# Optimization experiments

Hardware: AMD Instinct MI355X
Metric: run time of the kernel (lower is better)

## Reference

```python
import jax, jax.numpy as jnp
import numpy as np

TOP_K = 2


def setup_inputs() -> dict:
    key = jax.random.key(0)
    ks = jax.random.split(key, 8)
    B, S, D, I, E = 4, 2048, 1024, 2048, 8
    scale = 0.02
    return {
        "hidden_states": jax.random.normal(ks[0], (B, S, D), dtype=jnp.float32),
        "router_w": jax.random.normal(ks[1], (D, E), dtype=jnp.float32) * scale,
        "router_b": jnp.zeros((E,), dtype=jnp.float32),
        "gate_w": jax.random.normal(ks[2], (E, D, I), dtype=jnp.float32) * scale,
        "gate_b": jnp.zeros((E, I), dtype=jnp.float32),
        "up_w": jax.random.normal(ks[3], (E, D, I), dtype=jnp.float32) * scale,
        "up_b": jnp.zeros((E, I), dtype=jnp.float32),
        "down_w": jax.random.normal(ks[4], (E, I, D), dtype=jnp.float32) * scale,
        "down_b": jnp.zeros((E, D), dtype=jnp.float32),
    }


def reference(hidden_states, router_w, router_b, gate_w, gate_b, up_w, up_b, down_w, down_b):
    B, S, D = hidden_states.shape
    E = router_w.shape[1]
    x = hidden_states.reshape(-1, D)  # [T, D]
    T = x.shape[0]

    # Router: softmax over experts, then top-k selection + renormalization
    logits = x @ router_w + router_b              # [T, E]
    probs = jax.nn.softmax(logits, axis=-1)       # [T, E]
    top_v, top_i = jax.lax.top_k(probs, TOP_K)    # [T, K]
    top_v = top_v / jnp.sum(top_v, axis=-1, keepdims=True)

    # Scatter renormalized probs to dense [T, E] combine weights (top-k indices are distinct)
    weights = jnp.zeros((T, E), dtype=x.dtype).at[jnp.arange(T)[:, None], top_i].set(top_v)

    # Dense expert SwiGLU: compute all experts, weighted combine (faithful math)
    gate = jnp.einsum('td,edi->eti', x, gate_w) + gate_b[:, None, :]   # [E, T, I]
    up = jnp.einsum('td,edi->eti', x, up_w) + up_b[:, None, :]         # [E, T, I]
    h = jax.nn.silu(gate) * up                                          # [E, T, I]
    expert_out = jnp.einsum('eti,eid->etd', h, down_w) + down_b[:, None, :]  # [E, T, D]

    y = jnp.einsum('te,etd->td', weights, expert_out)                   # [T, D]
    return y.reshape(B, S, D)
```

## Files before the change

### kernel.cpp

```cpp
#include <hip/hip_runtime.h>

#define T_TOK 8192
#define DDIM 1024
#define IDIM 2048
#define NEXP 8

typedef short bf16x8 __attribute__((ext_vector_type(8)));
typedef float f32x4 __attribute__((ext_vector_type(4)));

__device__ __forceinline__ unsigned short f2bf(float f) {
  union { float f; unsigned int u; } v; v.f = f;
  unsigned int r = v.u + 0x7fffu + ((v.u >> 16) & 1u);
  return (unsigned short)(r >> 16);
}
__device__ __forceinline__ float bf2f(unsigned short u) {
  union { unsigned int u; float f; } v; v.u = (unsigned int)u << 16;
  return v.f;
}

typedef const __attribute__((address_space(1))) void* gas_t;
typedef __attribute__((address_space(3))) void* las_t;
__device__ __forceinline__ void async_copy16(void* lds, const void* g) {
  __builtin_amdgcn_global_load_lds((gas_t)g, (las_t)lds, 16, 0, 0);
}

__global__ __launch_bounds__(256) void tconv_kernel(
    const float* __restrict__ src, ushort* __restrict__ dst, int R, int C,
    int sel, int interleave, size_t srcEStride, size_t dstEStride) {
  __shared__ ushort lt[64 * 72];
  const int e = blockIdx.z;
  const float* s = src + (size_t)e * srcEStride;
  ushort* d = dst + (size_t)e * dstEStride;
  const int c0 = blockIdx.x * 64, r0 = blockIdx.y * 64;
  const int t = threadIdx.x;
  const int tr = t >> 2;
  const int tc = (t & 3) * 16;
  const float* sp = s + (size_t)(r0 + tr) * C + c0 + tc;
  float4 v0 = ((const float4*)sp)[0];
  float4 v1 = ((const float4*)sp)[1];
  float4 v2 = ((const float4*)sp)[2];
  float4 v3 = ((const float4*)sp)[3];
#pragma unroll
  for (int j = 0; j < 4; ++j) lt[(tc + j) * 72 + tr]      = f2bf(((const float*)&v0)[j]);
#pragma unroll
  for (int j = 0; j < 4; ++j) lt[(tc + 4 + j) * 72 + tr]  = f2bf(((const float*)&v1)[j]);
#pragma unroll
  for (int j = 0; j < 4; ++j) lt[(tc + 8 + j) * 72 + tr]  = f2bf(((const float*)&v2)[j]);
#pragma unroll
  for (int j = 0; j < 4; ++j) lt[(tc + 12 + j) * 72 + tr] = f2bf(((const float*)&v3)[j]);
  __syncthreads();
  const int cr = t >> 2;
  const int seg = (t & 3) * 16;
  const int ci = c0 + cr;
  const int drow = interleave ? ((ci >> 6) * 128 + sel * 64 + (ci & 63)) : ci;
  uint4 o0 = *(const uint4*)&lt[cr * 72 + seg];
  uint4 o1 = *(const uint4*)&lt[cr * 72 + seg + 8];
  ushort* dp = d + (size_t)drow * R + r0 + seg;
  *(uint4*)dp = o0;
  *(uint4*)(dp + 8) = o1;
}

__global__ __launch_bounds__(256) void router_kernel(
    const float* __restrict__ x, const float* __restrict__ rw, const float* __restrict__ rb,
    int* __restrict__ cnt, int* __restrict__ lists, float* __restrict__ wts,
    int* __restrict__ pexp, ushort* __restrict__ xb) {
  __shared__ int tokE[128];
  __shared__ int loc[128];
  __shared__ int hist[NEXP];
  __shared__ int base[NEXP];
  const int tid = threadIdx.x;
  const int w = tid >> 6, lane = tid & 63;
  if (tid < NEXP) hist[tid] = 0;
  __syncthreads();

#pragma unroll 1
  for (int tt = 0; tt < 16; ++tt) {
    const int token = blockIdx.x * 64 + w * 16 + tt;
    float acc[NEXP];
#pragma unroll
    for (int e = 0; e < NEXP; ++e) acc[e] = 0.f;
    const float* xr = x + (size_t)token * DDIM;
    ushort* xbr = xb + (size_t)token * DDIM;
#pragma unroll
    for (int j = 0; j < DDIM / 64; ++j) {
      int d = j * 64 + lane;
      float xv = xr[d];
      xbr[d] = f2bf(xv);
      const float4* wp = (const float4*)(rw + d * NEXP);
      float4 w0 = wp[0], w1 = wp[1];
      acc[0] += xv * w0.x; acc[1] += xv * w0.y; acc[2] += xv * w0.z; acc[3] += xv * w0.w;
      acc[4] += xv * w1.x; acc[5] += xv * w1.y; acc[6] += xv * w1.z; acc[7] += xv * w1.w;
    }
#pragma unroll
    for (int e = 0; e < NEXP; ++e) {
      float v = acc[e];
      for (int off = 32; off > 0; off >>= 1) v += __shfl_xor(v, off, 64);
      acc[e] = v;
    }
    if (lane == 0) {
      float l[NEXP];
#pragma unroll
      for (int e = 0; e < NEXP; ++e) l[e] = acc[e] + rb[e];
      int i0 = 0; float b0 = l[0];
#pragma unroll
      for (int e = 1; e < NEXP; ++e) if (l[e] > b0) { b0 = l[e]; i0 = e; }
      int i1 = -1; float b1 = -3.0e38f;
#pragma unroll
      for (int e = 0; e < NEXP; ++e) if (e != i0 && l[e] > b1) { b1 = l[e]; i1 = e; }
      float e1 = expf(b1 - b0);
      float inv = 1.f / (1.f + e1);
      wts[token * 2 + 0] = inv;
      wts[token * 2 + 1] = e1 * inv;
      pexp[token * 2 + 0] = i0;
      pexp[token * 2 + 1] = i1;
      const int k = (w * 16 + tt) * 2;
      tokE[k] = i0;
      tokE[k + 1] = i1;
      loc[k] = atomicAdd(&hist[i0], 1);
      loc[k + 1] = atomicAdd(&hist[i1], 1);
    }
  }
  __syncthreads();
  if (tid < NEXP) base[tid] = atomicAdd(&cnt[tid], hist[tid]);
  __syncthreads();
  if (tid < 128) {
    const int e = tokE[tid];
    const int token = blockIdx.x * 64 + (tid >> 1);
    lists[e * T_TOK + base[e] + loc[tid]] = token * 2 + (tid & 1);
  }
}

__global__ __launch_bounds__(256, 2) void gemm1_kernel(
    const ushort* __restrict__ xb, const ushort* __restrict__ wcat,
    const float* __restrict__ gate_b, const float* __restrict__ up_b,
    const int* __restrict__ lists, const int* __restrict__ cnt,
    ushort* __restrict__ hbuf) {
  const int e = blockIdx.z;
  const int ce = cnt[e];
  const int p = blockIdx.x + (blockIdx.y << 5);
  const int l = (p & 7) * 128 + (p >> 3);
  const int m0 = (l & 31) * 256;
  const int by = l >> 5;
  if (m0 >= ce) return;

  __shared__ __align__(16) ushort smem[256 * 64 + 128 * 64];
  __shared__ int rowinfo[256];
  ushort* As = smem;
  ushort* Bs = smem + 256 * 64;

  const int tid = threadIdx.x;
  {
    int slot = m0 + tid;
    rowinfo[tid] = lists[e * T_TOK + (slot < ce ? slot : 0)];
  }
  __syncthreads();

  const int w = tid >> 6, lane = tid & 63;
  const int fm = lane & 15, fq = lane >> 4;
  const int lr = lane >> 3;
  const int lchunk = ((lane & 7) ^ lr) * 8;

  const ushort* wcatE = wcat + (size_t)e * 4096 * 1024;
  const ushort* aG[8]; const ushort* bG[4];
  ushort* aL[8]; ushort* bL[4];
#pragma unroll
  for (int j = 0; j < 8; ++j) {
    int rl = 64 * w + 8 * j + lr;
    aG[j] = xb + (size_t)(rowinfo[rl] >> 1) * DDIM + lchunk;
    aL[j] = As + (64 * w + 8 * j) * 64;
  }
#pragma unroll
  for (int j = 0; j < 4; ++j) {
    int rl = 32 * w + 8 * j + lr;
    bG[j] = wcatE + (size_t)(128 * by + rl) * DDIM + lchunk;
    bL[j] = Bs + (32 * w + 8 * j) * 64;
  }

  f32x4 acc[4][8];
  const f32x4 zero4 = {0.f, 0.f, 0.f, 0.f};
#pragma unroll
  for (int i = 0; i < 4; ++i)
#pragma unroll
    for (int j = 0; j < 8; ++j) acc[i][j] = zero4;

#pragma unroll 1
  for (int kt = 0; kt < DDIM / 64; ++kt) {
    __syncthreads();
#pragma unroll
    for (int j = 0; j < 8; ++j) async_copy16(aL[j], aG[j] + kt * 64);
#pragma unroll
    for (int j = 0; j < 4; ++j) async_copy16(bL[j], bG[j] + kt * 64);
    __syncthreads();
#pragma unroll
    for (int ks = 0; ks < 2; ++ks) {
      bf16x8 af[4], bfr[8];
#pragma unroll
      for (int mf = 0; mf < 4; ++mf) {
        int row = 64 * w + 16 * mf + fm;
        af[mf] = *(const bf16x8*)&As[row * 64 + (((ks * 4 + fq) ^ (fm & 7)) * 8)];
      }
#pragma unroll
      for (int nf = 0; nf < 8; ++nf) {
        int row = 16 * nf + fm;
        bfr[nf] = *(const bf16x8*)&Bs[row * 64 + (((ks * 4 + fq) ^ (fm & 7)) * 8)];
      }
#pragma unroll
      for (int mf = 0; mf < 4; ++mf)
#pragma unroll
        for (int nf = 0; nf < 8; ++nf)
          acc[mf][nf] = __builtin_amdgcn_mfma_f32_16x16x32_bf16(af[mf], bfr[nf], acc[mf][nf], 0, 0, 0);
    }
  }

#pragma unroll
  for (int mf = 0; mf < 4; ++mf) {
#pragma unroll
    for (int r = 0; r < 4; ++r) {
      const int row = 64 * w + 16 * mf + 4 * fq + r;
      if (m0 + row < ce) {
        const int packed = rowinfo[row];
#pragma unroll
        for (int nf = 0; nf < 4; ++nf) {
          const int col = 64 * by + 16 * nf + fm;
          float g = acc[mf][nf][r] + gate_b[e * IDIM + col];
          float u = acc[mf][nf + 4][r] + up_b[e * IDIM + col];
          float h = g * (1.f / (1.f + __expf(-g))) * u;
          hbuf[(size_t)packed * IDIM + col] = f2bf(h);
        }
      }
    }
  }
}

__global__ __launch_bounds__(256, 2) void gemm2_kernel(
    const ushort* __restrict__ hbuf, const ushort* __restrict__ downT,
    const int* __restrict__ lists, const int* __restrict__ cnt,
    ushort* __restrict__ cbuf) {
  const int e = blockIdx.z;
  const int ce = cnt[e];
  const int p = blockIdx.x + (blockIdx.y << 5);
  const int l = (p & 7) * 32 + (p >> 3);
  const int m0 = (l & 31) * 256;
  const int by = l >> 5;
  if (m0 >= ce) return;

  __shared__ __align__(16) ushort smem[256 * 64 + 128 * 64];
  __shared__ int rowinfo[256];
  ushort* As = smem;
  ushort* Bs = smem + 256 * 64;

  const int tid = threadIdx.x;
  {
    int slot = m0 + tid;
    rowinfo[tid] = lists[e * T_TOK + (slot < ce ? slot : 0)];
  }
  __syncthreads();

  const int w = tid >> 6, lane = tid & 63;
  const int fm = lane & 15, fq = lane >> 4;
  const int lr = lane >> 3;
  const int lchunk = ((lane & 7) ^ lr) * 8;

  const ushort* downE = downT + (size_t)e * DDIM * IDIM;
  const ushort* aG[8]; const ushort* bG[4];
  ushort* aL[8]; ushort* bL[4];
#pragma unroll
  for (int j = 0; j < 8; ++j) {
    int rl = 64 * w + 8 * j + lr;
    aG[j] = hbuf + (size_t)rowinfo[rl] * IDIM + lchunk;
    aL[j] = As + (64 * w + 8 * j) * 64;
  }
#pragma unroll
  for (int j = 0; j < 4; ++j) {
    int rl = 32 * w + 8 * j + lr;
    bG[j] = downE + (size_t)(128 * by + rl) * IDIM + lchunk;
    bL[j] = Bs + (32 * w + 8 * j) * 64;
  }

  f32x4 acc[4][8];
  const f32x4 zero4 = {0.f, 0.f, 0.f, 0.f};
#pragma unroll
  for (int i = 0; i < 4; ++i)
#pragma unroll
    for (int j = 0; j < 8; ++j) acc[i][j] = zero4;

#pragma unroll 1
  for (int kt = 0; kt < IDIM / 64; ++kt) {
    __syncthreads();
#pragma unroll
    for (int j = 0; j < 8; ++j) async_copy16(aL[j], aG[j] + kt * 64);
#pragma unroll
    for (int j = 0; j < 4; ++j) async_copy16(bL[j], bG[j] + kt * 64);
    __syncthreads();
#pragma unroll
    for (int ks = 0; ks < 2; ++ks) {
      bf16x8 af[4], bfr[8];
#pragma unroll
      for (int mf = 0; mf < 4; ++mf) {
        int row = 64 * w + 16 * mf + fm;
        af[mf] = *(const bf16x8*)&As[row * 64 + (((ks * 4 + fq) ^ (fm & 7)) * 8)];
      }
#pragma unroll
      for (int nf = 0; nf < 8; ++nf) {
        int row = 16 * nf + fm;
        bfr[nf] = *(const bf16x8*)&Bs[row * 64 + (((ks * 4 + fq) ^ (fm & 7)) * 8)];
      }
#pragma unroll
      for (int mf = 0; mf < 4; ++mf)
#pragma unroll
        for (int nf = 0; nf < 8; ++nf)
          acc[mf][nf] = __builtin_amdgcn_mfma_f32_16x16x32_bf16(af[mf], bfr[nf], acc[mf][nf], 0, 0, 0);
    }
  }

#pragma unroll
  for (int mf = 0; mf < 4; ++mf) {
#pragma unroll
    for (int r = 0; r < 4; ++r) {
      const int row = 64 * w + 16 * mf + 4 * fq + r;
      if (m0 + row < ce) {
        const int packed = rowinfo[row];
        ushort* crow = cbuf + (size_t)packed * DDIM + 128 * by;
#pragma unroll
        for (int nf = 0; nf < 8; ++nf)
          crow[16 * nf + fm] = f2bf(acc[mf][nf][r]);
      }
    }
  }
}

__global__ __launch_bounds__(256) void combine_kernel(
    const ushort* __restrict__ cbuf, const float* __restrict__ down_b,
    const int* __restrict__ pexp, const float* __restrict__ wts,
    float* __restrict__ out) {
  const int i = blockIdx.x * 256 + threadIdx.x;
  const int token = i >> 7;
  const int seg = (i & 127) * 8;
  const float w0 = wts[token * 2], w1 = wts[token * 2 + 1];
  const int e0 = pexp[token * 2], e1 = pexp[token * 2 + 1];
  const ushort* c0 = cbuf + (size_t)(token * 2) * DDIM + seg;
  const ushort* c1 = c0 + DDIM;
  const float* b0 = down_b + e0 * DDIM + seg;
  const float* b1 = down_b + e1 * DDIM + seg;
  ushort4 v0a = ((const ushort4*)c0)[0], v0b = ((const ushort4*)c0)[1];
  ushort4 v1a = ((const ushort4*)c1)[0], v1b = ((const ushort4*)c1)[1];
  float4 ba0 = ((const float4*)b0)[0], bb0 = ((const float4*)b0)[1];
  float4 ba1 = ((const float4*)b1)[0], bb1 = ((const float4*)b1)[1];
  float4 o0, o1;
  o0.x = w0 * (bf2f(v0a.x) + ba0.x) + w1 * (bf2f(v1a.x) + ba1.x);
  o0.y = w0 * (bf2f(v0a.y) + ba0.y) + w1 * (bf2f(v1a.y) + ba1.y);
  o0.z = w0 * (bf2f(v0a.z) + ba0.z) + w1 * (bf2f(v1a.z) + ba1.z);
  o0.w = w0 * (bf2f(v0a.w) + ba0.w) + w1 * (bf2f(v1a.w) + ba1.w);
  o1.x = w0 * (bf2f(v0b.x) + bb0.x) + w1 * (bf2f(v1b.x) + bb1.x);
  o1.y = w0 * (bf2f(v0b.y) + bb0.y) + w1 * (bf2f(v1b.y) + bb1.y);
  o1.z = w0 * (bf2f(v0b.z) + bb0.z) + w1 * (bf2f(v1b.z) + bb1.z);
  o1.w = w0 * (bf2f(v0b.w) + bb0.w) + w1 * (bf2f(v1b.w) + bb1.w);
  float* op = out + (size_t)token * DDIM + seg;
  ((float4*)op)[0] = o0;
  ((float4*)op)[1] = o1;
}

extern "C" void kernel_launch(void* const* d_in, const int* in_sizes, int n_in,
                              void* d_out, int out_size, void* d_ws, size_t ws_size,
                              hipStream_t stream) {
  const float* x = (const float*)d_in[0];
  const float* rw = (const float*)d_in[1];
  const float* rb = (const float*)d_in[2];
  const float* gw = (const float*)d_in[3];
  const float* gb = (const float*)d_in[4];
  const float* uw = (const float*)d_in[5];
  const float* ub = (const float*)d_in[6];
  const float* dw = (const float*)d_in[7];
  const float* db = (const float*)d_in[8];
  float* out = (float*)d_out;

  char* ws = (char*)d_ws;
  ushort* xb    = (ushort*)(ws);
  ushort* hbuf  = (ushort*)(ws + (16ull << 20));
  ushort* wcat  = (ushort*)(ws + (80ull << 20));
  ushort* cbuf  = wcat;
  ushort* downT = (ushort*)(ws + (144ull << 20));
  float*  wts   = (float*) (ws + (176ull << 20));
  int*    lists = (int*)   (ws + (176ull << 20) + 65536);
  int*    cnt   = (int*)   (ws + (176ull << 20) + 65536 + 262144);
  int*    pexp  = (int*)   (ws + (176ull << 20) + 65536 + 262144 + 4096);

  hipMemsetAsync(cnt, 0, NEXP * sizeof(int), stream);

  router_kernel<<<T_TOK / 64, 256, 0, stream>>>(x, rw, rb, cnt, lists, wts, pexp, xb);
  tconv_kernel<<<dim3(IDIM / 64, DDIM / 64, NEXP), 256, 0, stream>>>(
      gw, wcat, DDIM, IDIM, 0, 1, (size_t)DDIM * IDIM, (size_t)2 * IDIM * DDIM);
  tconv_kernel<<<dim3(IDIM / 64, DDIM / 64, NEXP), 256, 0, stream>>>(
      uw, wcat, DDIM, IDIM, 1, 1, (size_t)DDIM * IDIM, (size_t)2 * IDIM * DDIM);
  tconv_kernel<<<dim3(DDIM / 64, IDIM / 64, NEXP), 256, 0, stream>>>(
      dw, downT, IDIM, DDIM, 0, 0, (size_t)IDIM * DDIM, (size_t)DDIM * IDIM);

  gemm1_kernel<<<dim3(32, 32, NEXP), 256, 0, stream>>>(
      xb, wcat, gb, ub, lists, cnt, hbuf);
  gemm2_kernel<<<dim3(32, 8, NEXP), 256, 0, stream>>>(
      hbuf, downT, lists, cnt, cbuf);
  combine_kernel<<<T_TOK * DDIM / 8 / 256, 256, 0, stream>>>(cbuf, db, pexp, wts, out);
}
```

Before: 577.1 us.

## Retile gemm1 to 128x128, fuse combine into gemm2 via atomics, merge tconv launches

Gemm1 moves from 256x128 tiles with one wave per 64 rows to 128x128 tiles split 2x2 across waves. Gate and up partial sums are exchanged through LDS, which halves accumulator registers and doubles the grid. The separate combine kernel is removed: gemm2 adds the bias, scales by the routing weight and atomically accumulates fp32 into a zeroed output, saving the bf16 intermediate round trip and one launch. The gate and up weight conversions are merged into one launch. The costs are fp32 atomics on 2x the output elements, an extra memset of the output, and an extra LDS exchange in the gemm1 epilogue.

```diff
diff --git a/kernel.cpp b/kernel.cpp
--- a/kernel.cpp
+++ b/kernel.cpp
@@ -26,10 +26,21 @@
 
 __global__ __launch_bounds__(256) void tconv_kernel(
     const float* __restrict__ src, ushort* __restrict__ dst, int R, int C,
-    int sel, int interleave, size_t srcEStride, size_t dstEStride) {
+    int zsel, int interleave, size_t srcEStride, size_t dstEStride,
+    const float* __restrict__ src2) {
   __shared__ ushort lt[64 * 72];
-  const int e = blockIdx.z;
-  const float* s = src + (size_t)e * srcEStride;
+  int e, sel;
+  const float* sbase;
+  if (zsel) {
+    e = blockIdx.z >> 1;
+    sel = blockIdx.z & 1;
+    sbase = sel ? src2 : src;
+  } else {
+    e = blockIdx.z;
+    sel = 0;
+    sbase = src;
+  }
+  const float* s = sbase + (size_t)e * srcEStride;
   ushort* d = dst + (size_t)e * dstEStride;
   const int c0 = blockIdx.x * 64, r0 = blockIdx.y * 64;
   const int t = threadIdx.x;
@@ -137,19 +148,19 @@
     ushort* __restrict__ hbuf) {
   const int e = blockIdx.z;
   const int ce = cnt[e];
-  const int p = blockIdx.x + (blockIdx.y << 5);
-  const int l = (p & 7) * 128 + (p >> 3);
-  const int m0 = (l & 31) * 256;
-  const int by = l >> 5;
+  const int p = blockIdx.x + (blockIdx.y << 6);
+  const int l = (p & 7) * 256 + (p >> 3);
+  const int m0 = (l & 63) * 128;
+  const int by = l >> 6;
   if (m0 >= ce) return;
 
-  __shared__ __align__(16) ushort smem[256 * 64 + 128 * 64];
-  __shared__ int rowinfo[256];
+  __shared__ __align__(16) ushort smem[2 * 128 * 64];
+  __shared__ int rowinfo[128];
   ushort* As = smem;
-  ushort* Bs = smem + 256 * 64;
+  ushort* Bs = smem + 128 * 64;
 
   const int tid = threadIdx.x;
-  {
+  if (tid < 128) {
     int slot = m0 + tid;
     rowinfo[tid] = lists[e * T_TOK + (slot < ce ? slot : 0)];
   }
@@ -157,75 +168,87 @@
 
   const int w = tid >> 6, lane = tid & 63;
   const int fm = lane & 15, fq = lane >> 4;
+  const int waveM = w >> 1, waveN = w & 1;
   const int lr = lane >> 3;
   const int lchunk = ((lane & 7) ^ lr) * 8;
 
   const ushort* wcatE = wcat + (size_t)e * 4096 * 1024;
-  const ushort* aG[8]; const ushort* bG[4];
-  ushort* aL[8]; ushort* bL[4];
-#pragma unroll
-  for (int j = 0; j < 8; ++j) {
-    int rl = 64 * w + 8 * j + lr;
-    aG[j] = xb + (size_t)(rowinfo[rl] >> 1) * DDIM + lchunk;
-    aL[j] = As + (64 * w + 8 * j) * 64;
-  }
+  const ushort* aG[4]; const ushort* bG[4];
+  ushort* aL[4]; ushort* bL[4];
 #pragma unroll
   for (int j = 0; j < 4; ++j) {
     int rl = 32 * w + 8 * j + lr;
+    aG[j] = xb + (size_t)(rowinfo[rl] >> 1) * DDIM + lchunk;
     bG[j] = wcatE + (size_t)(128 * by + rl) * DDIM + lchunk;
+    aL[j] = As + (32 * w + 8 * j) * 64;
     bL[j] = Bs + (32 * w + 8 * j) * 64;
   }
 
-  f32x4 acc[4][8];
+  f32x4 acc[4][4];
   const f32x4 zero4 = {0.f, 0.f, 0.f, 0.f};
 #pragma unroll
   for (int i = 0; i < 4; ++i)
 #pragma unroll
-    for (int j = 0; j < 8; ++j) acc[i][j] = zero4;
+    for (int j = 0; j < 4; ++j) acc[i][j] = zero4;
 
 #pragma unroll 1
   for (int kt = 0; kt < DDIM / 64; ++kt) {
     __syncthreads();
 #pragma unroll
-    for (int j = 0; j < 8; ++j) async_copy16(aL[j], aG[j] + kt * 64);
-#pragma unroll
-    for (int j = 0; j < 4; ++j) async_copy16(bL[j], bG[j] + kt * 64);
+    for (int j = 0; j < 4; ++j) {
+      async_copy16(aL[j], aG[j] + kt * 64);
+      async_copy16(bL[j], bG[j] + kt * 64);
+    }
     __syncthreads();
 #pragma unroll
     for (int ks = 0; ks < 2; ++ks) {
-      bf16x8 af[4], bfr[8];
+      bf16x8 af[4], bfr[4];
 #pragma unroll
       for (int mf = 0; mf < 4; ++mf) {
-        int row = 64 * w + 16 * mf + fm;
+        int row = 64 * waveM + 16 * mf + fm;
         af[mf] = *(const bf16x8*)&As[row * 64 + (((ks * 4 + fq) ^ (fm & 7)) * 8)];
       }
 #pragma unroll
-      for (int nf = 0; nf < 8; ++nf) {
-        int row = 16 * nf + fm;
+      for (int nf = 0; nf < 4; ++nf) {
+        int row = 64 * waveN + 16 * nf + fm;
         bfr[nf] = *(const bf16x8*)&Bs[row * 64 + (((ks * 4 + fq) ^ (fm & 7)) * 8)];
       }
 #pragma unroll
       for (int mf = 0; mf < 4; ++mf)
 #pragma unroll
-        for (int nf = 0; nf < 8; ++nf)
+        for (int nf = 0; nf < 4; ++nf)
           acc[mf][nf] = __builtin_amdgcn_mfma_f32_16x16x32_bf16(af[mf], bfr[nf], acc[mf][nf], 0, 0, 0);
     }
   }
 
-#pragma unroll
-  for (int mf = 0; mf < 4; ++mf) {
-#pragma unroll
-    for (int r = 0; r < 4; ++r) {
-      const int row = 64 * w + 16 * mf + 4 * fq + r;
-      if (m0 + row < ce) {
-        const int packed = rowinfo[row];
-#pragma unroll
-        for (int nf = 0; nf < 4; ++nf) {
-          const int col = 64 * by + 16 * nf + fm;
-          float g = acc[mf][nf][r] + gate_b[e * IDIM + col];
-          float u = acc[mf][nf + 4][r] + up_b[e * IDIM + col];
-          float h = g * (1.f / (1.f + __expf(-g))) * u;
-          hbuf[(size_t)packed * IDIM + col] = f2bf(h);
+  __syncthreads();
+  float* uld = (float*)smem;
+  if (waveN == 1) {
+#pragma unroll
+    for (int mf = 0; mf < 4; ++mf)
+#pragma unroll
+      for (int nf = 0; nf < 4; ++nf)
+#pragma unroll
+        for (int r = 0; r < 4; ++r)
+          uld[(64 * waveM + 16 * mf + 4 * fq + r) * 64 + 16 * nf + fm] = acc[mf][nf][r];
+  }
+  __syncthreads();
+  if (waveN == 0) {
+#pragma unroll
+    for (int mf = 0; mf < 4; ++mf) {
+#pragma unroll
+      for (int r = 0; r < 4; ++r) {
+        const int row = 64 * waveM + 16 * mf + 4 * fq + r;
+        if (m0 + row < ce) {
+          const int packed = rowinfo[row];
+#pragma unroll
+          for (int nf = 0; nf < 4; ++nf) {
+            const int col = 64 * by + 16 * nf + fm;
+            float g = acc[mf][nf][r] + gate_b[e * IDIM + col];
+            float u = uld[row * 64 + 16 * nf + fm] + up_b[e * IDIM + col];
+            float h = g * (1.f / (1.f + __expf(-g))) * u;
+            hbuf[(size_t)packed * IDIM + col] = f2bf(h);
+          }
         }
       }
     }
@@ -235,7 +258,8 @@
 __global__ __launch_bounds__(256, 2) void gemm2_kernel(
     const ushort* __restrict__ hbuf, const ushort* __restrict__ downT,
     const int* __restrict__ lists, const int* __restrict__ cnt,
-    ushort* __restrict__ cbuf) {
+    const float* __restrict__ down_b, const float* __restrict__ wts,
+    float* __restrict__ out) {
   const int e = blockIdx.z;
   const int ce = cnt[e];
   const int p = blockIdx.x + (blockIdx.y << 5);
@@ -313,6 +337,9 @@
     }
   }
 
+  float bias[8];
+#pragma unroll
+  for (int nf = 0; nf < 8; ++nf) bias[nf] = down_b[e * DDIM + 128 * by + 16 * nf + fm];
 #pragma unroll
   for (int mf = 0; mf < 4; ++mf) {
 #pragma unroll
@@ -320,44 +347,14 @@
       const int row = 64 * w + 16 * mf + 4 * fq + r;
       if (m0 + row < ce) {
         const int packed = rowinfo[row];
-        ushort* crow = cbuf + (size_t)packed * DDIM + 128 * by;
+        const float wgt = wts[packed];
+        float* orow = out + (size_t)(packed >> 1) * DDIM + 128 * by;
 #pragma unroll
         for (int nf = 0; nf < 8; ++nf)
-          crow[16 * nf + fm] = f2bf(acc[mf][nf][r]);
-      }
-    }
-  }
-}
-
-__global__ __launch_bounds__(256) void combine_kernel(
-    const ushort* __restrict__ cbuf, const float* __restrict__ down_b,
-    const int* __restrict__ pexp, const float* __restrict__ wts,
-    float* __restrict__ out) {
-  const int i = blockIdx.x * 256 + threadIdx.x;
-  const int token = i >> 7;
-  const int seg = (i & 127) * 8;
-  const float w0 = wts[token * 2], w1 = wts[token * 2 + 1];
-  const int e0 = pexp[token * 2], e1 = pexp[token * 2 + 1];
-  const ushort* c0 = cbuf + (size_t)(token * 2) * DDIM + seg;
-  const ushort* c1 = c0 + DDIM;
-  const float* b0 = down_b + e0 * DDIM + seg;
-  const float* b1 = down_b + e1 * DDIM + seg;
-  ushort4 v0a = ((const ushort4*)c0)[0], v0b = ((const ushort4*)c0)[1];
-  ushort4 v1a = ((const ushort4*)c1)[0], v1b = ((const ushort4*)c1)[1];
-  float4 ba0 = ((const float4*)b0)[0], bb0 = ((const float4*)b0)[1];
-  float4 ba1 = ((const float4*)b1)[0], bb1 = ((const float4*)b1)[1];
-  float4 o0, o1;
-  o0.x = w0 * (bf2f(v0a.x) + ba0.x) + w1 * (bf2f(v1a.x) + ba1.x);
-  o0.y = w0 * (bf2f(v0a.y) + ba0.y) + w1 * (bf2f(v1a.y) + ba1.y);
-  o0.z = w0 * (bf2f(v0a.z) + ba0.z) + w1 * (bf2f(v1a.z) + ba1.z);
-  o0.w = w0 * (bf2f(v0a.w) + ba0.w) + w1 * (bf2f(v1a.w) + ba1.w);
-  o1.x = w0 * (bf2f(v0b.x) + bb0.x) + w1 * (bf2f(v1b.x) + bb1.x);
-  o1.y = w0 * (bf2f(v0b.y) + bb0.y) + w1 * (bf2f(v1b.y) + bb1.y);
-  o1.z = w0 * (bf2f(v0b.z) + bb0.z) + w1 * (bf2f(v1b.z) + bb1.z);
-  o1.w = w0 * (bf2f(v0b.w) + bb0.w) + w1 * (bf2f(v1b.w) + bb1.w);
-  float* op = out + (size_t)token * DDIM + seg;
-  ((float4*)op)[0] = o0;
-  ((float4*)op)[1] = o1;
+          atomicAdd(&orow[16 * nf + fm], wgt * (acc[mf][nf][r] + bias[nf]));
+      }
+    }
+  }
 }
 
 extern "C" void kernel_launch(void* const* d_in, const int* in_sizes, int n_in,
@@ -378,7 +375,6 @@
   ushort* xb    = (ushort*)(ws);
   ushort* hbuf  = (ushort*)(ws + (16ull << 20));
   ushort* wcat  = (ushort*)(ws + (80ull << 20));
-  ushort* cbuf  = wcat;
   ushort* downT = (ushort*)(ws + (144ull << 20));
   float*  wts   = (float*) (ws + (176ull << 20));
   int*    lists = (int*)   (ws + (176ull << 20) + 65536);
@@ -386,18 +382,16 @@
   int*    pexp  = (int*)   (ws + (176ull << 20) + 65536 + 262144 + 4096);
 
   hipMemsetAsync(cnt, 0, NEXP * sizeof(int), stream);
+  hipMemsetAsync(out, 0, (size_t)T_TOK * DDIM * sizeof(float), stream);
 
   router_kernel<<<T_TOK / 64, 256, 0, stream>>>(x, rw, rb, cnt, lists, wts, pexp, xb);
-  tconv_kernel<<<dim3(IDIM / 64, DDIM / 64, NEXP), 256, 0, stream>>>(
-      gw, wcat, DDIM, IDIM, 0, 1, (size_t)DDIM * IDIM, (size_t)2 * IDIM * DDIM);
-  tconv_kernel<<<dim3(IDIM / 64, DDIM / 64, NEXP), 256, 0, stream>>>(
-      uw, wcat, DDIM, IDIM, 1, 1, (size_t)DDIM * IDIM, (size_t)2 * IDIM * DDIM);
+  tconv_kernel<<<dim3(IDIM / 64, DDIM / 64, NEXP * 2), 256, 0, stream>>>(
+      gw, wcat, DDIM, IDIM, 1, 1, (size_t)DDIM * IDIM, (size_t)2 * IDIM * DDIM, uw);
   tconv_kernel<<<dim3(DDIM / 64, IDIM / 64, NEXP), 256, 0, stream>>>(
-      dw, downT, IDIM, DDIM, 0, 0, (size_t)IDIM * DDIM, (size_t)DDIM * IDIM);
-
-  gemm1_kernel<<<dim3(32, 32, NEXP), 256, 0, stream>>>(
+      dw, downT, IDIM, DDIM, 0, 0, (size_t)IDIM * DDIM, (size_t)DDIM * IDIM, nullptr);
+
+  gemm1_kernel<<<dim3(T_TOK / 128, IDIM / 64, NEXP), 256, 0, stream>>>(
       xb, wcat, gb, ub, lists, cnt, hbuf);
   gemm2_kernel<<<dim3(32, 8, NEXP), 256, 0, stream>>>(
-      hbuf, downT, lists, cnt, cbuf);
-  combine_kernel<<<T_TOK * DDIM / 8 / 256, 256, 0, stream>>>(cbuf, db, pexp, wts, out);
-}
+      hbuf, downT, lists, cnt, db, wts, out);
+}
```

Measured after the change: 613.6 us. +6.3%, slower.
